# Kernel optimization log

Hardware: AMD Instinct MI355X
Metric: run time of the kernel (lower is better)

Reference implementation:

```python
import jax, jax.numpy as jnp
import numpy as np

D_MODEL, N_HEADS, D_FF = 1024, 16, 4096
B, L, PREFIX = 2, 2048, 512
EPS = 1e-5


def _ln(x, w, b):
    mu = jnp.mean(x, axis=-1, keepdims=True)
    var = jnp.mean((x - mu) ** 2, axis=-1, keepdims=True)
    return (x - mu) * jax.lax.rsqrt(var + EPS) * w + b


def setup_inputs() -> dict:
    key = jax.random.key(0)
    ks = jax.random.split(key, 5)
    d, f = D_MODEL, D_FF
    return {
        "x": jax.random.normal(ks[0], (B, L, d), jnp.float32),
        "ln1_w": jnp.ones((d,), jnp.float32),
        "ln1_b": jnp.zeros((d,), jnp.float32),
        "in_proj_w": jax.random.normal(ks[1], (3 * d, d), jnp.float32) / np.sqrt(d),
        "in_proj_b": jnp.zeros((3 * d,), jnp.float32),
        "out_w": jax.random.normal(ks[2], (d, d), jnp.float32) / np.sqrt(d),
        "out_b": jnp.zeros((d,), jnp.float32),
        "ln2_w": jnp.ones((d,), jnp.float32),
        "ln2_b": jnp.zeros((d,), jnp.float32),
        "fc1_w": jax.random.normal(ks[3], (f, d), jnp.float32) / np.sqrt(d),
        "fc1_b": jnp.zeros((f,), jnp.float32),
        "fc2_w": jax.random.normal(ks[4], (d, f), jnp.float32) / np.sqrt(f),
        "fc2_b": jnp.zeros((d,), jnp.float32),
        "prefix_len": PREFIX,
    }


def reference(x, ln1_w, ln1_b, in_proj_w, in_proj_b, out_w, out_b,
              ln2_w, ln2_b, fc1_w, fc1_b, fc2_w, fc2_b, prefix_len):
    Bv, Lv, d = x.shape
    H = N_HEADS
    hd = d // H
    m = prefix_len

    # additive prefix-decoder mask (L, L): allowed if j < m, or (i >= m and j <= i)
    i = jnp.arange(Lv)[:, None]
    j = jnp.arange(Lv)[None, :]
    allowed = (j < m) | ((i >= m) & (j <= i))
    mask = jnp.where(allowed, 0.0, -jnp.inf).astype(x.dtype)

    h = _ln(x, ln1_w, ln1_b)
    qkv = h @ in_proj_w.T + in_proj_b                      # [B, L, 3d]
    q, k, v = jnp.split(qkv, 3, axis=-1)
    q = q.reshape(Bv, Lv, H, hd)
    k = k.reshape(Bv, Lv, H, hd)
    v = v.reshape(Bv, Lv, H, hd)
    scale = 1.0 / np.sqrt(hd)
    scores = jnp.einsum("bihd,bjhd->bhij", q, k) * scale   # [B, H, L, L]
    attn = jax.nn.softmax(scores + mask, axis=-1)
    ctx = jnp.einsum("bhij,bjhd->bihd", attn, v).reshape(Bv, Lv, d)
    sa = ctx @ out_w.T + out_b
    x = x + sa

    h = _ln(x, ln2_w, ln2_b)
    ff = jax.nn.gelu(h @ fc1_w.T + fc1_b, approximate=False) @ fc2_w.T + fc2_b
    return x + ff
```

## Files before the change

### kernel.cpp

```cpp
#include <hip/hip_runtime.h>
#include <cstdint>
#include <cstddef>

#define DM   1024
#define NH   16
#define HD   64
#define DFF  4096
#define BB   2
#define LL   2048
#define MM   (BB*LL)

using short8 = __attribute__((ext_vector_type(8))) short;
using f32x4  = __attribute__((ext_vector_type(4))) float;

__device__ __forceinline__ unsigned short f2bf(float f) {
  union { float f; uint32_t u; } v; v.f = f;
  uint32_t u = v.u;
  uint32_t r = (u + 0x7fffu + ((u >> 16) & 1u)) >> 16;
  return (unsigned short)r;
}

__device__ __forceinline__ uint32_t cvtpk_bf16(float a, float b) {
  uint32_t r;
  asm("v_cvt_pk_bf16_f32 %0, %1, %2" : "=v"(r) : "v"(a), "v"(b));
  return r;
}

__device__ __forceinline__ float exp2_fast(float x) {
  float r;
  asm("v_exp_f32 %0, %1" : "=v"(r) : "v"(x));
  return r;
}

__device__ __forceinline__ float rcp_fast(float x) {
  float r;
  asm("v_rcp_f32 %0, %1" : "=v"(r) : "v"(x));
  return r;
}

#define GLDS16(gp, lp) \
  __builtin_amdgcn_global_load_lds((const __attribute__((address_space(1))) uint32_t*)(gp), \
                                   (__attribute__((address_space(3))) uint32_t*)(lp), 16, 0, 0)

__global__ __launch_bounds__(256) void convert_f32_bf16(const float* __restrict__ in,
                                                        unsigned short* __restrict__ out, int n4) {
  int i = blockIdx.x * 256 + threadIdx.x;
  if (i < n4) {
    float4 v = ((const float4*)in)[i];
    ushort4 o;
    o.x = f2bf(v.x); o.y = f2bf(v.y); o.z = f2bf(v.z); o.w = f2bf(v.w);
    ((ushort4*)out)[i] = o;
  }
}

__global__ __launch_bounds__(256) void ln_kernel(const float* __restrict__ x,
                                                 const float* __restrict__ w,
                                                 const float* __restrict__ b,
                                                 unsigned short* __restrict__ out) {
  int row = blockIdx.x, t = threadIdx.x;
  float4 v = ((const float4*)(x + (size_t)row * DM))[t];
  float s  = v.x + v.y + v.z + v.w;
  float sq = v.x*v.x + v.y*v.y + v.z*v.z + v.w*v.w;
  #pragma unroll
  for (int o = 32; o; o >>= 1) { s += __shfl_down(s, o); sq += __shfl_down(sq, o); }
  __shared__ float sh[8];
  if ((t & 63) == 0) { sh[t >> 6] = s; sh[4 + (t >> 6)] = sq; }
  __syncthreads();
  float S  = sh[0] + sh[1] + sh[2] + sh[3];
  float SQ = sh[4] + sh[5] + sh[6] + sh[7];
  float mu  = S * (1.0f / DM);
  float var = SQ * (1.0f / DM) - mu * mu;
  float rs  = rsqrtf(var + 1e-5f);
  float4 wv = ((const float4*)w)[t];
  float4 bv = ((const float4*)b)[t];
  ushort4 o;
  o.x = f2bf((v.x - mu) * rs * wv.x + bv.x);
  o.y = f2bf((v.y - mu) * rs * wv.y + bv.y);
  o.z = f2bf((v.z - mu) * rs * wv.z + bv.z);
  o.w = f2bf((v.w - mu) * rs * wv.w + bv.w);
  ((ushort4*)(out + (size_t)row * DM))[t] = o;
}

template <int EPI, int BM>
__global__ __launch_bounds__(256) void gemm_bt(const unsigned short* __restrict__ A,
                                               const unsigned short* __restrict__ Bw,
                                               const float* __restrict__ bias,
                                               const float* __restrict__ res,
                                               void* __restrict__ Cout,
                                               int M, int N, int K, int lda, int ldb) {
  constexpr int MI   = BM / 32;
  constexpr int ABUF = BM * 64;
  __shared__ unsigned short As[2 * ABUF];
  __shared__ unsigned short Bs[2 * 64 * 64];
  const int t = threadIdx.x;
  const int l = t & 63, lr = l & 15, lg = l >> 4;
  const int w = t >> 6, wm = w >> 1, wn = w & 1;

  int bx = blockIdx.x, by = blockIdx.y;
  {
    const int gx = gridDim.x;
    const int total = gx * gridDim.y;
    if ((total & 7) == 0) {
      int lin = by * gx + bx;
      int lin2 = (lin & 7) * (total >> 3) + (lin >> 3);
      bx = lin2 % gx;
      by = lin2 / gx;
    }
  }
  const int m0 = by * BM, n0 = bx * 64;

  f32x4 acc[MI][2];
  #pragma unroll
  for (int mi = 0; mi < MI; ++mi)
    #pragma unroll
    for (int ni = 0; ni < 2; ++ni) acc[mi][ni] = {0.f, 0.f, 0.f, 0.f};

  const int rowt = t >> 3, sw = (t & 7) ^ (rowt & 7);
  const unsigned short* Ag = A  + (size_t)(m0 + rowt) * lda + sw * 8;
  const unsigned short* Bg = Bw + (size_t)(n0 + rowt) * ldb + sw * 8;
  char* AsB = (char*)As + t * 16;
  char* BsB = (char*)Bs + t * 16;
  const size_t r32A = (size_t)32 * lda;
  const size_t r32B = (size_t)32 * ldb;

  const int rs = lr & 7;
  const int segA = (lg ^ rs) * 8;
  const int segB = ((lg + 4) ^ rs) * 8;

  #pragma unroll
  for (int g = 0; g < MI; ++g) GLDS16(Ag + g * r32A, AsB + g * 4096);
  GLDS16(Bg,        BsB);
  GLDS16(Bg + r32B, BsB + 4096);

  int cur = 0;
  for (int k0 = 0; k0 < K; k0 += 64, cur ^= 1) {
    __syncthreads();
    const int kn = k0 + 64;
    if (kn < K) {
      char* An = AsB + (cur ^ 1) * (ABUF * 2);
      char* Bn = BsB + (cur ^ 1) * 8192;
      #pragma unroll
      for (int g = 0; g < MI; ++g) GLDS16(Ag + kn + g * r32A, An + g * 4096);
      GLDS16(Bg + kn,        Bn);
      GLDS16(Bg + kn + r32B, Bn + 4096);
    }
    const unsigned short* Ab = As + cur * ABUF;
    const unsigned short* Bb = Bs + cur * (64 * 64);
    short8 af[MI][2], bfr[2][2];
    #pragma unroll
    for (int mi = 0; mi < MI; ++mi) {
      const int row = wm * (BM / 2) + mi * 16 + lr;
      af[mi][0] = *(const short8*)&Ab[row * 64 + segA];
      af[mi][1] = *(const short8*)&Ab[row * 64 + segB];
    }
    #pragma unroll
    for (int ni = 0; ni < 2; ++ni) {
      const int row = wn * 32 + ni * 16 + lr;
      bfr[ni][0] = *(const short8*)&Bb[row * 64 + segA];
      bfr[ni][1] = *(const short8*)&Bb[row * 64 + segB];
    }
    #pragma unroll
    for (int mi = 0; mi < MI; ++mi)
      #pragma unroll
      for (int ni = 0; ni < 2; ++ni) {
        acc[mi][ni] = __builtin_amdgcn_mfma_f32_16x16x32_bf16(af[mi][0], bfr[ni][0], acc[mi][ni], 0, 0, 0);
        acc[mi][ni] = __builtin_amdgcn_mfma_f32_16x16x32_bf16(af[mi][1], bfr[ni][1], acc[mi][ni], 0, 0, 0);
      }
  }

  #pragma unroll
  for (int mi = 0; mi < MI; ++mi) {
    int row = m0 + wm * (BM / 2) + mi * 16 + lg * 4;
    #pragma unroll
    for (int ni = 0; ni < 2; ++ni) {
      int col = n0 + wn * 32 + ni * 16 + lr;
      float bv = (EPI == 3) ? 0.f : bias[col];
      #pragma unroll
      for (int r = 0; r < 4; ++r) {
        float v = acc[mi][ni][r] + bv;
        size_t idx = (size_t)(row + r) * N + col;
        if (EPI == 0) {
          ((unsigned short*)Cout)[idx] = f2bf(v);
        } else if (EPI == 1) {
          ((float*)Cout)[idx] = res[idx] + v;
        } else if (EPI == 2) {
          float y = v * (0.7978845608028654f + 0.035677408136300125f * v * v);
          float e = exp2_fast(y * 2.885390081777927f);
          float tnh = 1.0f - 2.0f * rcp_fast(1.0f + e);
          float g = 0.5f * v * (1.0f + tnh);
          ((unsigned short*)Cout)[idx] = f2bf(g);
        } else {
          ((float*)Cout)[idx] += v;
        }
      }
    }
  }
}

__global__ __launch_bounds__(256) void vtrans_kernel(const unsigned short* __restrict__ qkv,
                                                     unsigned short* __restrict__ vt) {
  __shared__ unsigned short tile[64][72];
  int bh = blockIdx.y, b = bh >> 4, h = bh & 15;
  int j0 = blockIdx.x * 64, t = threadIdx.x;
  #pragma unroll
  for (int r = 0; r < 2; ++r) {
    int j = r * 32 + (t >> 3), d0 = (t & 7) * 8;
    short8 v = *(const short8*)(qkv + (size_t)(b * LL + j0 + j) * 3072 + 2048 + h * 64 + d0);
    #pragma unroll
    for (int e = 0; e < 8; ++e) tile[j][d0 + e] = (unsigned short)v[e];
  }
  __syncthreads();
  #pragma unroll
  for (int r = 0; r < 2; ++r) {
    int d = r * 32 + (t >> 3), j = (t & 7) * 8;
    short8 o;
    #pragma unroll
    for (int e = 0; e < 8; ++e) o[e] = (short)tile[j + e][d];
    *(short8*)(vt + (size_t)(bh * 64 + d) * LL + j0 + j) = o;
  }
}

__global__ __launch_bounds__(512) void attn_kernel(const unsigned short* __restrict__ qkv,
                                                   const unsigned short* __restrict__ vt,
                                                   const int* __restrict__ prefix,
                                                   unsigned short* __restrict__ ctx) {
  __shared__ unsigned short Ks[2][64 * 64];
  __shared__ unsigned short Vs[2][64 * 64];
  __shared__ unsigned short Plds[8][16][72];
  const int t = threadIdx.x, w = t >> 6, l = t & 63, lr = l & 15, lg = l >> 4;
  const int bh = blockIdx.y, b = bh >> 4, h = bh & 15;
  const int ib = gridDim.x - 1 - blockIdx.x;
  const int i0 = ib * 128, iw = i0 + w * 16;
  const int m = *prefix;
  const float C = 0.125f * 1.44269504088896f;

  const int r0 = t >> 3, s0 = t & 7, swz = s0 ^ (r0 & 7);
  const unsigned short* Kg0 = qkv + (size_t)(b * LL + r0) * 3072 + DM + h * 64 + swz * 8;
  const unsigned short* Vg0 = vt + (size_t)(bh * 64 + r0) * LL + swz * 8;
  char* KdB = (char*)Ks + t * 16;
  char* VdB = (char*)Vs + t * 16;
  const int rs = lr & 7;
  const int segA = (lg ^ rs) * 8;
  const int segB = ((lg + 4) ^ rs) * 8;

  short8 qf[2];
  {
    const unsigned short* qrow = qkv + (size_t)(b * LL + iw + lr) * 3072 + h * 64;
    qf[0] = *(const short8*)(qrow + lg * 8);
    qf[1] = *(const short8*)(qrow + 32 + lg * 8);
  }
  short8 ones;
  #pragma unroll
  for (int e = 0; e < 8; ++e) ones[e] = (short)0x3F80;

  f32x4 Ot[4];
  #pragma unroll
  for (int dt = 0; dt < 4; ++dt) Ot[dt] = {0.f, 0.f, 0.f, 0.f};
  f32x4 Osum = {0.f, 0.f, 0.f, 0.f};

  const int jmax = (i0 + 128 <= m) ? m : (i0 + 128);
  const int nb = (jmax + 63) >> 6;
  const int i_abs = iw + lr;

  GLDS16(Kg0, KdB);
  GLDS16(Vg0, VdB);

  for (int c = 0; c < nb; ++c) {
    __syncthreads();
    if (c + 1 < nb) {
      const size_t jn = (size_t)(c + 1) * 64;
      const int pn = (c + 1) & 1;
      GLDS16(Kg0 + jn * 3072, KdB + pn * 8192);
      GLDS16(Vg0 + jn,        VdB + pn * 8192);
    }
    const int jt = c * 64, p = c & 1;

    f32x4 sc[4];
    #pragma unroll
    for (int nt = 0; nt < 4; ++nt) {
      sc[nt] = {0.f, 0.f, 0.f, 0.f};
      const int row = nt * 16 + lr;
      short8 kf0 = *(const short8*)&Ks[p][row * 64 + segA];
      short8 kf1 = *(const short8*)&Ks[p][row * 64 + segB];
      sc[nt] = __builtin_amdgcn_mfma_f32_16x16x32_bf16(kf0, qf[0], sc[nt], 0, 0, 0);
      sc[nt] = __builtin_amdgcn_mfma_f32_16x16x32_bf16(kf1, qf[1], sc[nt], 0, 0, 0);
    }
    const bool full = (jt + 64 <= m) || (iw >= m && jt + 64 <= iw + 1);
    #pragma unroll
    for (int nt = 0; nt < 4; ++nt) {
      float p0 = exp2_fast(sc[nt][0] * C);
      float p1 = exp2_fast(sc[nt][1] * C);
      float p2 = exp2_fast(sc[nt][2] * C);
      float p3 = exp2_fast(sc[nt][3] * C);
      if (!full) {
        const int jb = jt + nt * 16 + lg * 4;
        const bool causal_i = (i_abs >= m);
        p0 = ((jb + 0 < m) || (causal_i && jb + 0 <= i_abs)) ? p0 : 0.f;
        p1 = ((jb + 1 < m) || (causal_i && jb + 1 <= i_abs)) ? p1 : 0.f;
        p2 = ((jb + 2 < m) || (causal_i && jb + 2 <= i_abs)) ? p2 : 0.f;
        p3 = ((jb + 3 < m) || (causal_i && jb + 3 <= i_abs)) ? p3 : 0.f;
      }
      uint2 pk;
      pk.x = cvtpk_bf16(p0, p1);
      pk.y = cvtpk_bf16(p2, p3);
      *(uint2*)&Plds[w][lr][nt * 16 + lg * 4] = pk;
    }
    short8 paf0 = *(const short8*)&Plds[w][lr][lg * 8];
    short8 paf1 = *(const short8*)&Plds[w][lr][32 + lg * 8];
    #pragma unroll
    for (int dt = 0; dt < 4; ++dt) {
      const int row = dt * 16 + lr;
      short8 vf0 = *(const short8*)&Vs[p][row * 64 + segA];
      short8 vf1 = *(const short8*)&Vs[p][row * 64 + segB];
      Ot[dt] = __builtin_amdgcn_mfma_f32_16x16x32_bf16(paf0, vf0, Ot[dt], 0, 0, 0);
      Ot[dt] = __builtin_amdgcn_mfma_f32_16x16x32_bf16(paf1, vf1, Ot[dt], 0, 0, 0);
    }
    Osum = __builtin_amdgcn_mfma_f32_16x16x32_bf16(paf0, ones, Osum, 0, 0, 0);
    Osum = __builtin_amdgcn_mfma_f32_16x16x32_bf16(paf1, ones, Osum, 0, 0, 0);
  }
  #pragma unroll
  for (int r = 0; r < 4; ++r) {
    float inv = 1.0f / Osum[r];
    size_t row = (size_t)(b * LL + iw + lg * 4 + r);
    #pragma unroll
    for (int dt = 0; dt < 4; ++dt)
      ctx[row * DM + h * 64 + dt * 16 + lr] = f2bf(Ot[dt][r] * inv);
  }
}

extern "C" void kernel_launch(void* const* d_in, const int* in_sizes, int n_in,
                              void* d_out, int out_size, void* d_ws, size_t ws_size,
                              hipStream_t stream) {
  const float* x        = (const float*)d_in[0];
  const float* ln1_w    = (const float*)d_in[1];
  const float* ln1_b    = (const float*)d_in[2];
  const float* in_proj_w= (const float*)d_in[3];
  const float* in_proj_b= (const float*)d_in[4];
  const float* out_w    = (const float*)d_in[5];
  const float* out_b    = (const float*)d_in[6];
  const float* ln2_w    = (const float*)d_in[7];
  const float* ln2_b    = (const float*)d_in[8];
  const float* fc1_w    = (const float*)d_in[9];
  const float* fc1_b    = (const float*)d_in[10];
  const float* fc2_w    = (const float*)d_in[11];
  const float* fc2_b    = (const float*)d_in[12];
  const int*   prefix   = (const int*)d_in[13];
  float* outp = (float*)d_out;

  char* ws = (char*)d_ws;
  unsigned short* slab  = (unsigned short*)ws;
  float*          x2    = (float*)(ws + ((size_t)8 << 20));
  unsigned short* vtb   = (unsigned short*)(ws + ((size_t)8 << 20));
  unsigned short* wslab = (unsigned short*)(ws + ((size_t)24 << 20));
  unsigned short* qkv   = (unsigned short*)(ws + ((size_t)32 << 20));
  unsigned short* wfc2  = (unsigned short*)(ws + ((size_t)32 << 20));
  unsigned short* ffh   = (unsigned short*)(ws + ((size_t)40 << 20));
  const bool big = ws_size >= ((size_t)72 << 20);

  convert_f32_bf16<<<3072, 256, 0, stream>>>(in_proj_w, wslab, 3072 * 1024 / 4);
  ln_kernel<<<MM, 256, 0, stream>>>(x, ln1_w, ln1_b, slab);
  gemm_bt<0, 128><<<dim3(3072 / 64, MM / 128), 256, 0, stream>>>(slab, wslab, in_proj_b, nullptr, qkv, MM, 3072, 1024, 1024, 1024);
  vtrans_kernel<<<dim3(LL / 64, BB * NH), 256, 0, stream>>>(qkv, vtb);
  attn_kernel<<<dim3(LL / 128, BB * NH), 512, 0, stream>>>(qkv, vtb, prefix, slab);
  convert_f32_bf16<<<1024, 256, 0, stream>>>(out_w, wslab, 1024 * 1024 / 4);
  gemm_bt<1, 64><<<dim3(1024 / 64, MM / 64), 256, 0, stream>>>(slab, wslab, out_b, x, x2, MM, 1024, 1024, 1024, 1024);

  ln_kernel<<<MM, 256, 0, stream>>>(x2, ln2_w, ln2_b, slab);
  convert_f32_bf16<<<4096, 256, 0, stream>>>(fc1_w, wslab, 4096 * 1024 / 4);
  convert_f32_bf16<<<4096, 256, 0, stream>>>(fc2_w, wfc2, 1024 * 4096 / 4);
  if (big) {
    unsigned short* ffmid = (unsigned short*)(ws + ((size_t)40 << 20));
    gemm_bt<2, 128><<<dim3(4096 / 64, MM / 128), 256, 0, stream>>>(slab, wslab, fc1_b, nullptr, ffmid, MM, 4096, 1024, 1024, 1024);
    gemm_bt<1, 64><<<dim3(1024 / 64, MM / 64), 256, 0, stream>>>(ffmid, wfc2, fc2_b, x2, outp, MM, 1024, 4096, 4096, 4096);
  } else {
    gemm_bt<2, 128><<<dim3(2048 / 64, MM / 128), 256, 0, stream>>>(slab, wslab, fc1_b, nullptr, ffh, MM, 2048, 1024, 1024, 1024);
    gemm_bt<1, 64><<<dim3(1024 / 64, MM / 64), 256, 0, stream>>>(ffh, wfc2, fc2_b, x2, outp, MM, 1024, 2048, 2048, 4096);
    gemm_bt<2, 128><<<dim3(2048 / 64, MM / 128), 256, 0, stream>>>(slab, wslab + (size_t)2048 * 1024, fc1_b + 2048, nullptr, ffh, MM, 2048, 1024, 1024, 1024);
    gemm_bt<3, 64><<<dim3(1024 / 64, MM / 64), 256, 0, stream>>>(ffh, wfc2 + 2048, nullptr, nullptr, outp, MM, 1024, 2048, 2048, 4096);
  }
}
```

Measured before the change: 243.2 us.

## Add 256x256-tile 8-wave GEMM for QKV and FC1 projections

Result: faster. 229.5 us (-5.6%).

```diff
diff --git a/kernel.cpp b/kernel.cpp
--- a/kernel.cpp
+++ b/kernel.cpp
@@ -36,6 +36,13 @@
   float r;
   asm("v_rcp_f32 %0, %1" : "=v"(r) : "v"(x));
   return r;
+}
+
+__device__ __forceinline__ float gelu_tanh(float v) {
+  float y = v * (0.7978845608028654f + 0.035677408136300125f * v * v);
+  float e = exp2_fast(y * 2.885390081777927f);
+  float tnh = 1.0f - 2.0f * rcp_fast(1.0f + e);
+  return 0.5f * v * (1.0f + tnh);
 }
 
 #define GLDS16(gp, lp) \
@@ -81,6 +88,128 @@
   ((ushort4*)(out + (size_t)row * DM))[t] = o;
 }
 
+template <int EPI>
+__global__ __launch_bounds__(512) void gemm8(const unsigned short* __restrict__ A,
+                                             const unsigned short* __restrict__ Bw,
+                                             const float* __restrict__ bias,
+                                             unsigned short* __restrict__ Cout,
+                                             int M, int N, int K, int lda, int ldb) {
+  __shared__ unsigned short As[2 * 256 * 64];
+  __shared__ unsigned short Bs[2 * 256 * 64];
+  const int t = threadIdx.x;
+  const int l = t & 63, lr = l & 15, lg = l >> 4;
+  const int wid = t >> 6, wm = wid >> 2, wn = wid & 3;
+
+  int bx = blockIdx.x, by = blockIdx.y;
+  {
+    const int gx = gridDim.x;
+    const int total = gx * gridDim.y;
+    if ((total & 7) == 0) {
+      int lin = by * gx + bx;
+      int lin2 = (lin & 7) * (total >> 3) + (lin >> 3);
+      bx = lin2 % gx;
+      by = lin2 / gx;
+    }
+  }
+  const int m0 = by * 256, n0 = bx * 256;
+
+  f32x4 acc[8][4];
+  #pragma unroll
+  for (int mi = 0; mi < 8; ++mi)
+    #pragma unroll
+    for (int ni = 0; ni < 4; ++ni) acc[mi][ni] = {0.f, 0.f, 0.f, 0.f};
+
+  const int rowt = t >> 3, sw = (t & 7) ^ (rowt & 7);
+  const unsigned short* Ag = A  + (size_t)(m0 + rowt) * lda + sw * 8;
+  const unsigned short* Bg = Bw + (size_t)(n0 + rowt) * ldb + sw * 8;
+  const size_t r64A = (size_t)64 * lda;
+  const size_t r64B = (size_t)64 * ldb;
+
+  const int rs = lr & 7;
+  const int segA = (lg ^ rs) * 8;
+  const int segB = ((lg + 4) ^ rs) * 8;
+
+  const int nt = K >> 6;
+
+  auto stage = [&](int kt, int buf) {
+    const int k0 = kt << 6;
+    char* Ad = (char*)As + buf * 32768 + t * 16;
+    char* Bd = (char*)Bs + buf * 32768 + t * 16;
+    #pragma unroll
+    for (int g = 0; g < 4; ++g) GLDS16(Ag + k0 + g * r64A, Ad + g * 8192);
+    #pragma unroll
+    for (int g = 0; g < 4; ++g) GLDS16(Bg + k0 + g * r64B, Bd + g * 8192);
+  };
+
+  stage(0, 0);
+  stage(1, 1);
+
+  for (int kt = 0; kt < nt; ++kt) {
+    const int cur = kt & 1;
+    if (kt + 1 < nt) {
+      asm volatile("s_waitcnt vmcnt(8)" ::: "memory");
+    } else {
+      asm volatile("s_waitcnt vmcnt(0)" ::: "memory");
+    }
+    __builtin_amdgcn_s_barrier();
+    asm volatile("" ::: "memory");
+
+    const unsigned short* Ab = As + cur * 16384;
+    const unsigned short* Bb = Bs + cur * 16384;
+    short8 bfr[4][2];
+    #pragma unroll
+    for (int ni = 0; ni < 4; ++ni) {
+      const int row = wn * 64 + ni * 16 + lr;
+      bfr[ni][0] = *(const short8*)&Bb[row * 64 + segA];
+      bfr[ni][1] = *(const short8*)&Bb[row * 64 + segB];
+    }
+    __builtin_amdgcn_s_setprio(1);
+    #pragma unroll
+    for (int mp = 0; mp < 4; ++mp) {
+      short8 af[2][2];
+      #pragma unroll
+      for (int q = 0; q < 2; ++q) {
+        const int row = wm * 128 + (mp * 2 + q) * 16 + lr;
+        af[q][0] = *(const short8*)&Ab[row * 64 + segA];
+        af[q][1] = *(const short8*)&Ab[row * 64 + segB];
+      }
+      #pragma unroll
+      for (int q = 0; q < 2; ++q)
+        #pragma unroll
+        for (int ni = 0; ni < 4; ++ni) {
+          acc[mp * 2 + q][ni] = __builtin_amdgcn_mfma_f32_16x16x32_bf16(af[q][0], bfr[ni][0], acc[mp * 2 + q][ni], 0, 0, 0);
+          acc[mp * 2 + q][ni] = __builtin_amdgcn_mfma_f32_16x16x32_bf16(af[q][1], bfr[ni][1], acc[mp * 2 + q][ni], 0, 0, 0);
+        }
+    }
+    __builtin_amdgcn_s_setprio(0);
+
+    asm volatile("" ::: "memory");
+    __builtin_amdgcn_s_barrier();
+    asm volatile("" ::: "memory");
+    if (kt + 2 < nt) stage(kt + 2, cur);
+  }
+
+  #pragma unroll
+  for (int mi = 0; mi < 8; ++mi) {
+    int row = m0 + wm * 128 + mi * 16 + lg * 4;
+    #pragma unroll
+    for (int ni = 0; ni < 4; ++ni) {
+      int col = n0 + wn * 64 + ni * 16 + lr;
+      float bv = bias[col];
+      #pragma unroll
+      for (int r = 0; r < 4; ++r) {
+        float v = acc[mi][ni][r] + bv;
+        size_t idx = (size_t)(row + r) * N + col;
+        if (EPI == 0) {
+          Cout[idx] = f2bf(v);
+        } else {
+          Cout[idx] = f2bf(gelu_tanh(v));
+        }
+      }
+    }
+  }
+}
+
 template <int EPI, int BM>
 __global__ __launch_bounds__(256) void gemm_bt(const unsigned short* __restrict__ A,
                                                const unsigned short* __restrict__ Bw,
@@ -184,11 +313,7 @@
         } else if (EPI == 1) {
           ((float*)Cout)[idx] = res[idx] + v;
         } else if (EPI == 2) {
-          float y = v * (0.7978845608028654f + 0.035677408136300125f * v * v);
-          float e = exp2_fast(y * 2.885390081777927f);
-          float tnh = 1.0f - 2.0f * rcp_fast(1.0f + e);
-          float g = 0.5f * v * (1.0f + tnh);
-          ((unsigned short*)Cout)[idx] = f2bf(g);
+          ((unsigned short*)Cout)[idx] = f2bf(gelu_tanh(v));
         } else {
           ((float*)Cout)[idx] += v;
         }
@@ -359,7 +484,7 @@
 
   convert_f32_bf16<<<3072, 256, 0, stream>>>(in_proj_w, wslab, 3072 * 1024 / 4);
   ln_kernel<<<MM, 256, 0, stream>>>(x, ln1_w, ln1_b, slab);
-  gemm_bt<0, 128><<<dim3(3072 / 64, MM / 128), 256, 0, stream>>>(slab, wslab, in_proj_b, nullptr, qkv, MM, 3072, 1024, 1024, 1024);
+  gemm8<0><<<dim3(3072 / 256, MM / 256), 512, 0, stream>>>(slab, wslab, in_proj_b, qkv, MM, 3072, 1024, 1024, 1024);
   vtrans_kernel<<<dim3(LL / 64, BB * NH), 256, 0, stream>>>(qkv, vtb);
   attn_kernel<<<dim3(LL / 128, BB * NH), 512, 0, stream>>>(qkv, vtb, prefix, slab);
   convert_f32_bf16<<<1024, 256, 0, stream>>>(out_w, wslab, 1024 * 1024 / 4);
@@ -370,7 +495,7 @@
   convert_f32_bf16<<<4096, 256, 0, stream>>>(fc2_w, wfc2, 1024 * 4096 / 4);
   if (big) {
     unsigned short* ffmid = (unsigned short*)(ws + ((size_t)40 << 20));
-    gemm_bt<2, 128><<<dim3(4096 / 64, MM / 128), 256, 0, stream>>>(slab, wslab, fc1_b, nullptr, ffmid, MM, 4096, 1024, 1024, 1024);
+    gemm8<2><<<dim3(4096 / 256, MM / 256), 512, 0, stream>>>(slab, wslab, fc1_b, ffmid, MM, 4096, 1024, 1024, 1024);
     gemm_bt<1, 64><<<dim3(1024 / 64, MM / 64), 256, 0, stream>>>(ffmid, wfc2, fc2_b, x2, outp, MM, 1024, 4096, 4096, 4096);
   } else {
     gemm_bt<2, 128><<<dim3(2048 / 64, MM / 128), 256, 0, stream>>>(slab, wslab, fc1_b, nullptr, ffh, MM, 2048, 1024, 1024, 1024);
```
